# Kernel tuning notes

Hardware: AMD Instinct MI355X
Metric: run time of the kernel (lower is better)

## Reference

```python
import jax, jax.numpy as jnp
import numpy as np

TOP_K = 5


def setup_inputs() -> dict:
    key = jax.random.key(0)
    k1, k2 = jax.random.split(key)
    batch, n_attr, feat_dim = 4096, 64000, 512  # 1000 classes x 64 attrs
    image_features = jax.random.normal(k1, (batch, feat_dim), dtype=jnp.float32)
    # raw (unnormalized) attribute concept features, flattened to (n_attr, feat_dim)
    attr_features = jax.random.normal(k2, (n_attr, feat_dim), dtype=jnp.float32)
    return {"image_features": image_features, "attr_features": attr_features}


def reference(image_features, attr_features):
    # __init__: L2-normalize attribute features along feature dim
    attr_norm = attr_features / jnp.linalg.norm(attr_features, axis=-1, keepdims=True)
    # similarities: (batch, n_attr) dense dot-product matrix
    similarities = image_features @ attr_norm.T
    # top-k along attribute dim
    top_scores, top_indices = jax.lax.top_k(similarities, TOP_K)
    # gather selected attribute vectors: (batch, top_k, feat_dim)
    top_attr_features = attr_norm[top_indices]
    return (top_attr_features, top_scores)
```

## Files before the change

kernel.cpp:

```cpp
#include <hip/hip_runtime.h>
#include <float.h>

#define FEAT 512
#define TOPK 5
#define NSEL 16
#define BM 256
#define BN 256
#define BKT 64
#define NKT (FEAT / BKT)
#define ABYTES (BM * BKT)
#define BUFB (2 * ABYTES)
#define NCB 4

typedef __attribute__((ext_vector_type(4))) int i32x4;

__device__ __forceinline__ void gl_lds16(const void* g, void* lds) {
    __builtin_amdgcn_global_load_lds(
        (const __attribute__((address_space(1))) unsigned int*)g,
        (__attribute__((address_space(3))) unsigned int*)lds, 16, 0, 0);
}

__global__ __launch_bounds__(256) void quant_attr(
    const float* __restrict__ in, signed char* __restrict__ q,
    float* __restrict__ inv) {
    const int w = threadIdx.x >> 6, l = threadIdx.x & 63;
    const int row = blockIdx.x * 4 + w;
    const float4* p = reinterpret_cast<const float4*>(in) + (size_t)row * (FEAT / 4);
    const float4 v0 = p[l * 2], v1 = p[l * 2 + 1];
    float ss = v0.x * v0.x + v0.y * v0.y + v0.z * v0.z + v0.w * v0.w +
               v1.x * v1.x + v1.y * v1.y + v1.z * v1.z + v1.w * v1.w;
#pragma unroll
    for (int m = 1; m < 64; m <<= 1) ss += __shfl_xor(ss, m);
    const float iv = 1.0f / sqrtf(fmaxf(ss, 1e-30f));
    const float qs = iv * 300.0f;
    int qv[8];
    qv[0] = __float2int_rn(v0.x * qs); qv[1] = __float2int_rn(v0.y * qs);
    qv[2] = __float2int_rn(v0.z * qs); qv[3] = __float2int_rn(v0.w * qs);
    qv[4] = __float2int_rn(v1.x * qs); qv[5] = __float2int_rn(v1.y * qs);
    qv[6] = __float2int_rn(v1.z * qs); qv[7] = __float2int_rn(v1.w * qs);
#pragma unroll
    for (int j = 0; j < 8; ++j) qv[j] = min(127, max(-127, qv[j]));
    int2 st;
    st.x = (qv[0] & 255) | ((qv[1] & 255) << 8) | ((qv[2] & 255) << 16) |
           ((unsigned)(qv[3] & 255) << 24);
    st.y = (qv[4] & 255) | ((qv[5] & 255) << 8) | ((qv[6] & 255) << 16) |
           ((unsigned)(qv[7] & 255) << 24);
    *reinterpret_cast<int2*>(q + (size_t)row * FEAT + l * 8) = st;
    if (l == 0) inv[row] = iv;
}

__global__ __launch_bounds__(256) void quant_img(
    const float* __restrict__ in, signed char* __restrict__ q) {
    const int w = threadIdx.x >> 6, l = threadIdx.x & 63;
    const int row = blockIdx.x * 4 + w;
    const float4* p = reinterpret_cast<const float4*>(in) + (size_t)row * (FEAT / 4);
    const float4 v0 = p[l * 2], v1 = p[l * 2 + 1];
    float mx = fmaxf(fmaxf(fmaxf(fabsf(v0.x), fabsf(v0.y)), fmaxf(fabsf(v0.z), fabsf(v0.w))),
                     fmaxf(fmaxf(fabsf(v1.x), fabsf(v1.y)), fmaxf(fabsf(v1.z), fabsf(v1.w))));
#pragma unroll
    for (int m = 1; m < 64; m <<= 1) mx = fmaxf(mx, __shfl_xor(mx, m));
    mx = fmaxf(mx, 1e-20f);
    const float qs = 127.0f / mx;
    const int q0 = __float2int_rn(v0.x * qs), q1 = __float2int_rn(v0.y * qs);
    const int q2 = __float2int_rn(v0.z * qs), q3 = __float2int_rn(v0.w * qs);
    const int q4 = __float2int_rn(v1.x * qs), q5 = __float2int_rn(v1.y * qs);
    const int q6 = __float2int_rn(v1.z * qs), q7 = __float2int_rn(v1.w * qs);
    int2 st;
    st.x = (q0 & 255) | ((q1 & 255) << 8) | ((q2 & 255) << 16) | ((unsigned)(q3 & 255) << 24);
    st.y = (q4 & 255) | ((q5 & 255) << 8) | ((q6 & 255) << 16) | ((unsigned)(q7 & 255) << 24);
    *reinterpret_cast<int2*>(q + (size_t)row * FEAT + l * 8) = st;
}

__global__ __launch_bounds__(512, 2) void coarse_kernel(
    const signed char* __restrict__ attrQ, const signed char* __restrict__ imgQ,
    unsigned* __restrict__ cand, int nablk, int niblk) {
    __shared__ __align__(1024) char lds[3][BUFB];
    const int tid = threadIdx.x;

    const int cpx = gridDim.x >> 3;
    const int wg = ((int)blockIdx.x & 7) * cpx + ((int)blockIdx.x >> 3);
    const int ablock = wg / niblk;
    const int iblock = wg % niblk;

    const int w = tid >> 6, l = tid & 63;
    const int wr = w >> 2, wc = w & 3;
    const int lrow = l & 15, lg = l >> 4;

    const int srow = tid >> 2, sg = tid & 3;
    const int ssw = sg ^ ((srow ^ (srow >> 2)) & 3);
    const signed char* asrc = attrQ + (size_t)(ablock * BM + srow) * FEAT + (ssw << 4);
    const signed char* bsrc = imgQ + (size_t)(iblock * BN + srow) * FEAT + (ssw << 4);

    int a_off[8], b_off[4];
#pragma unroll
    for (int m = 0; m < 8; ++m) {
        const int r = wr * 128 + m * 16 + lrow;
        a_off[m] = r * BKT + ((lg ^ ((r ^ (r >> 2)) & 3)) << 4);
    }
#pragma unroll
    for (int n = 0; n < 4; ++n) {
        const int r = wc * 64 + n * 16 + lrow;
        b_off[n] = ABYTES + r * BKT + ((lg ^ ((r ^ (r >> 2)) & 3)) << 4);
    }

    i32x4 acc[8][4];
#pragma unroll
    for (int m = 0; m < 8; ++m)
#pragma unroll
        for (int n = 0; n < 4; ++n) acc[m][n] = (i32x4){0, 0, 0, 0};

#define STAGE(bufi, kt)                                                      \
    {                                                                        \
        char* d_ = &lds[bufi][tid * 16];                                     \
        gl_lds16(asrc + (kt) * BKT, d_);                                     \
        gl_lds16(asrc + (kt) * BKT + (size_t)128 * FEAT, d_ + 8192);         \
        gl_lds16(bsrc + (kt) * BKT, d_ + 16384);                             \
        gl_lds16(bsrc + (kt) * BKT + (size_t)128 * FEAT, d_ + 24576);        \
    }

    STAGE(0, 0);
    int cur = 0, nxt = 1;
#pragma unroll 1
    for (int t = 0; t < NKT; ++t) {
        if (t < NKT - 1) {
            STAGE(nxt, t + 1);
            asm volatile("s_waitcnt vmcnt(4)" ::: "memory");
        } else {
            asm volatile("s_waitcnt vmcnt(0)" ::: "memory");
        }
        __builtin_amdgcn_s_barrier();
        __builtin_amdgcn_sched_barrier(0);
        const char* buf = &lds[cur][0];
        i32x4 bF[4], aF[8];
#pragma unroll
        for (int n = 0; n < 4; ++n)
            bF[n] = *reinterpret_cast<const i32x4*>(buf + b_off[n]);
#pragma unroll
        for (int m = 0; m < 8; ++m)
            aF[m] = *reinterpret_cast<const i32x4*>(buf + a_off[m]);
        __builtin_amdgcn_s_setprio(1);
#pragma unroll
        for (int m = 0; m < 8; ++m)
#pragma unroll
            for (int n = 0; n < 4; ++n)
                acc[m][n] = __builtin_amdgcn_mfma_i32_16x16x64_i8(
                    aF[m], bF[n], acc[m][n], 0, 0, 0);
        __builtin_amdgcn_s_setprio(0);
        cur = (cur == 2) ? 0 : cur + 1;
        nxt = (nxt == 2) ? 0 : nxt + 1;
    }
#undef STAGE

    unsigned m1[4] = {0u, 0u, 0u, 0u}, m2[4] = {0u, 0u, 0u, 0u};
#pragma unroll
    for (int m = 0; m < 8; ++m)
#pragma unroll
        for (int r = 0; r < 4; ++r) {
            const int rowl = wr * 128 + m * 16 + lg * 4 + r;
            const unsigned idxc = 2047u - (unsigned)rowl;
#pragma unroll
            for (int n = 0; n < 4; ++n) {
                const unsigned p =
                    (((unsigned)(acc[m][n][r] + (1 << 23)) << 8) & 0xFFFFF800u) | idxc;
                m2[n] = max(m2[n], min(m1[n], p));
                m1[n] = max(m1[n], p);
            }
        }

    unsigned* scratch = reinterpret_cast<unsigned*>(&lds[0][0]);
#pragma unroll
    for (int n = 0; n < 4; ++n) {
        scratch[(w * 64 + l) * 8 + n * 2] = m1[n];
        scratch[(w * 64 + l) * 8 + n * 2 + 1] = m2[n];
    }
    __syncthreads();

    if (tid < BN) {
        const int wc2 = tid >> 6, cw = tid & 63;
        const int n = cw >> 4, lr = cw & 15;
        unsigned best[NCB] = {0u, 0u, 0u, 0u};
#pragma unroll
        for (int wr2 = 0; wr2 < 2; ++wr2)
#pragma unroll
            for (int lg2 = 0; lg2 < 4; ++lg2)
#pragma unroll
                for (int k = 0; k < 2; ++k) {
                    const unsigned p =
                        scratch[((wr2 * 4 + wc2) * 64 + lg2 * 16 + lr) * 8 + n * 2 + k];
                    if (p > best[NCB - 1]) {
                        best[NCB - 1] = p;
#pragma unroll
                        for (int x = NCB - 1; x > 0; --x)
                            if (best[x] > best[x - 1]) {
                                const unsigned t_ = best[x];
                                best[x] = best[x - 1]; best[x - 1] = t_;
                            }
                    }
                }
        const size_t base = ((size_t)(iblock * BN + tid) * nablk + ablock) * NCB;
#pragma unroll
        for (int j = 0; j < NCB; ++j) cand[base + j] = best[j];
    }
}

__global__ __launch_bounds__(64) void select16_kernel(
    const unsigned* __restrict__ cand, int* __restrict__ sel, int nablk) {
    const int row = blockIdx.x;
    const int l = threadIdx.x;
    const int ncand = nablk * NCB;
    const unsigned* cr = cand + (size_t)row * ncand;
    unsigned p[16]; int c[16];
#pragma unroll
    for (int j = 0; j < 16; ++j) {
        const int slot = l * 16 + j;
        if (slot < ncand) {
            const unsigned v = cr[slot];
            p[j] = v;
            c[j] = (slot / NCB) * BM + (2047 - (int)(v & 0x7FFu));
        } else { p[j] = 0u; c[j] = 0x7fffffff; }
    }
    int* out = sel + (size_t)row * NSEL;
    for (int r = 0; r < NSEL; ++r) {
        unsigned bp = 0u; int bc = 0x7fffffff;
#pragma unroll
        for (int j = 0; j < 16; ++j)
            if (p[j] > bp || (p[j] == bp && c[j] < bc)) { bp = p[j]; bc = c[j]; }
#pragma unroll
        for (int m = 1; m < 64; m <<= 1) {
            const unsigned op = __shfl_xor(bp, m);
            const int oc = __shfl_xor(bc, m);
            if (op > bp || (op == bp && oc < bc)) { bp = op; bc = oc; }
        }
        if (l == 0) out[r] = bc;
#pragma unroll
        for (int j = 0; j < 16; ++j)
            if (p[j] == bp && c[j] == bc) { p[j] = 0u; c[j] = 0x7fffffff; }
    }
}

__global__ __launch_bounds__(256) void rescore_kernel(
    const float* __restrict__ img, const float* __restrict__ attr,
    const float* __restrict__ inv, const int* __restrict__ sel,
    float* __restrict__ out_scores, int* __restrict__ final_i) {
    __shared__ float s_sc[NSEL];
    const int row = blockIdx.x;
    const int w = threadIdx.x >> 6, l = threadIdx.x & 63;
    const float4* ip = reinterpret_cast<const float4*>(img) + (size_t)row * (FEAT / 4);
    const float4 a0 = ip[l * 2], a1 = ip[l * 2 + 1];
#pragma unroll
    for (int q = 0; q < 4; ++q) {
        const int slot = w * 4 + q;
        const int ci = sel[(size_t)row * NSEL + slot];
        const float4* ap = reinterpret_cast<const float4*>(attr) + (size_t)ci * (FEAT / 4);
        const float4 b0 = ap[l * 2], b1 = ap[l * 2 + 1];
        float d = a0.x * b0.x + a0.y * b0.y + a0.z * b0.z + a0.w * b0.w +
                  a1.x * b1.x + a1.y * b1.y + a1.z * b1.z + a1.w * b1.w;
#pragma unroll
        for (int m = 1; m < 64; m <<= 1) d += __shfl_xor(d, m);
        if (l == 0) s_sc[slot] = d * inv[ci];
    }
    __syncthreads();
    if (threadIdx.x == 0) {
        float ts[TOPK]; int ti[TOPK];
#pragma unroll
        for (int j = 0; j < TOPK; ++j) { ts[j] = -FLT_MAX; ti[j] = 0x7fffffff; }
        for (int e = 0; e < NSEL; ++e) {
            const float sv = s_sc[e];
            const int iv = sel[(size_t)row * NSEL + e];
            if (sv > ts[4] || (sv == ts[4] && iv < ti[4])) {
                ts[4] = sv; ti[4] = iv;
#pragma unroll
                for (int x = 4; x > 0; --x)
                    if (ts[x] > ts[x - 1] || (ts[x] == ts[x - 1] && ti[x] < ti[x - 1])) {
                        const float tf = ts[x]; ts[x] = ts[x - 1]; ts[x - 1] = tf;
                        const int td = ti[x]; ti[x] = ti[x - 1]; ti[x - 1] = td;
                    }
            }
        }
#pragma unroll
        for (int j = 0; j < TOPK; ++j) {
            out_scores[(size_t)row * TOPK + j] = ts[j];
            final_i[(size_t)row * TOPK + j] = ti[j];
        }
    }
}

__global__ __launch_bounds__(128) void gather_kernel(
    const float* __restrict__ attr, const float* __restrict__ inv,
    const int* __restrict__ final_i, float* __restrict__ out0) {
    const int pair = blockIdx.x;
    const int fi = final_i[pair];
    const float sc = inv[fi];
    const float4 v =
        reinterpret_cast<const float4*>(attr)[(size_t)fi * (FEAT / 4) + threadIdx.x];
    float4 o;
    o.x = v.x * sc; o.y = v.y * sc; o.z = v.z * sc; o.w = v.w * sc;
    reinterpret_cast<float4*>(out0)[(size_t)pair * (FEAT / 4) + threadIdx.x] = o;
}

extern "C" void kernel_launch(void* const* d_in, const int* in_sizes, int n_in,
                              void* d_out, int out_size, void* d_ws, size_t ws_size,
                              hipStream_t stream) {
    const float* img = (const float*)d_in[0];
    const float* attr = (const float*)d_in[1];
    const int batch = in_sizes[0] / FEAT;
    const int nattr = in_sizes[1] / FEAT;
    const int nablk = nattr / BM;
    const int niblk = batch / BN;

    char* ws = (char*)d_ws;
    signed char* attrQ = (signed char*)ws; ws += (size_t)nattr * FEAT;
    signed char* imgQ = (signed char*)ws;  ws += (size_t)batch * FEAT;
    float* inv = (float*)ws;               ws += (size_t)nattr * 4;
    unsigned* cand = (unsigned*)ws;        ws += (size_t)batch * nablk * NCB * 4;
    int* sel = (int*)ws;                   ws += (size_t)batch * NSEL * 4;
    int* final_i = (int*)ws;               ws += (size_t)batch * TOPK * 4;

    float* out0 = (float*)d_out;
    float* out_scores = out0 + (size_t)batch * TOPK * FEAT;

    quant_attr<<<nattr / 4, 256, 0, stream>>>(attr, attrQ, inv);
    quant_img<<<batch / 4, 256, 0, stream>>>(img, imgQ);
    coarse_kernel<<<nablk * niblk, 512, 0, stream>>>(attrQ, imgQ, cand, nablk, niblk);
    select16_kernel<<<batch, 64, 0, stream>>>(cand, sel, nablk);
    rescore_kernel<<<batch, 256, 0, stream>>>(img, attr, inv, sel, out_scores, final_i);
    gather_kernel<<<batch * TOPK, 128, 0, stream>>>(attr, inv, final_i, out0);
}
```

Baseline: 282.2 us.

## Switch coarse GEMM to 32x32x32 int8 MFMA and fuse select/rescore/gather kernels

The coarse int8 GEMM now uses 32x32x32 MFMA tiles instead of 16x16x64, which cuts the number of MFMA issues and LDS fragment reads per k-step. Its LDS staging drops from triple to double buffering, with an extra barrier after each k-step, and a cross-half shuffle is added to the per-column top-2 reduction. Separately, the select16, rescore and gather kernels are merged into one per-row kernel that keeps the selected indices in shared memory, removing two launches and the global intermediates. The extra barrier may expose more load latency in the GEMM loop.

```diff
diff --git a/kernel.cpp b/kernel.cpp
--- a/kernel.cpp
+++ b/kernel.cpp
@@ -8,11 +8,12 @@
 #define BN 256
 #define BKT 64
 #define NKT (FEAT / BKT)
-#define ABYTES (BM * BKT)
-#define BUFB (2 * ABYTES)
+#define A_BYTES (BM * BKT)
+#define BUFB (2 * A_BYTES)
 #define NCB 4
 
 typedef __attribute__((ext_vector_type(4))) int i32x4;
+typedef __attribute__((ext_vector_type(16))) int i32x16;
 
 __device__ __forceinline__ void gl_lds16(const void* g, void* lds) {
     __builtin_amdgcn_global_load_lds(
@@ -74,7 +75,7 @@
 __global__ __launch_bounds__(512, 2) void coarse_kernel(
     const signed char* __restrict__ attrQ, const signed char* __restrict__ imgQ,
     unsigned* __restrict__ cand, int nablk, int niblk) {
-    __shared__ __align__(1024) char lds[3][BUFB];
+    __shared__ __align__(1024) char lds[2][BUFB];
     const int tid = threadIdx.x;
 
     const int cpx = gridDim.x >> 3;
@@ -84,30 +85,38 @@
 
     const int w = tid >> 6, l = tid & 63;
     const int wr = w >> 2, wc = w & 3;
-    const int lrow = l & 15, lg = l >> 4;
+    const int l31 = l & 31, lh = l >> 5;
 
     const int srow = tid >> 2, sg = tid & 3;
     const int ssw = sg ^ ((srow ^ (srow >> 2)) & 3);
     const signed char* asrc = attrQ + (size_t)(ablock * BM + srow) * FEAT + (ssw << 4);
     const signed char* bsrc = imgQ + (size_t)(iblock * BN + srow) * FEAT + (ssw << 4);
 
-    int a_off[8], b_off[4];
-#pragma unroll
-    for (int m = 0; m < 8; ++m) {
-        const int r = wr * 128 + m * 16 + lrow;
-        a_off[m] = r * BKT + ((lg ^ ((r ^ (r >> 2)) & 3)) << 4);
-    }
-#pragma unroll
-    for (int n = 0; n < 4; ++n) {
-        const int r = wc * 64 + n * 16 + lrow;
-        b_off[n] = ABYTES + r * BKT + ((lg ^ ((r ^ (r >> 2)) & 3)) << 4);
-    }
-
-    i32x4 acc[8][4];
-#pragma unroll
-    for (int m = 0; m < 8; ++m)
-#pragma unroll
-        for (int n = 0; n < 4; ++n) acc[m][n] = (i32x4){0, 0, 0, 0};
+    int a_off[4][2], b_off[2][2];
+#pragma unroll
+    for (int m = 0; m < 4; ++m)
+#pragma unroll
+        for (int ks = 0; ks < 2; ++ks) {
+            const int r = wr * 128 + m * 32 + l31;
+            const int g = ks * 2 + lh;
+            a_off[m][ks] = r * BKT + ((g ^ ((r ^ (r >> 2)) & 3)) << 4);
+        }
+#pragma unroll
+    for (int n = 0; n < 2; ++n)
+#pragma unroll
+        for (int ks = 0; ks < 2; ++ks) {
+            const int r = wc * 64 + n * 32 + l31;
+            const int g = ks * 2 + lh;
+            b_off[n][ks] = A_BYTES + r * BKT + ((g ^ ((r ^ (r >> 2)) & 3)) << 4);
+        }
+
+    i32x16 acc[4][2];
+#pragma unroll
+    for (int m = 0; m < 4; ++m)
+#pragma unroll
+        for (int n = 0; n < 2; ++n)
+#pragma unroll
+            for (int e = 0; e < 16; ++e) acc[m][n][e] = 0;
 
 #define STAGE(bufi, kt)                                                      \
     {                                                                        \
@@ -119,11 +128,11 @@
     }
 
     STAGE(0, 0);
-    int cur = 0, nxt = 1;
+    int cur = 0;
 #pragma unroll 1
     for (int t = 0; t < NKT; ++t) {
         if (t < NKT - 1) {
-            STAGE(nxt, t + 1);
+            STAGE(cur ^ 1, t + 1);
             asm volatile("s_waitcnt vmcnt(4)" ::: "memory");
         } else {
             asm volatile("s_waitcnt vmcnt(0)" ::: "memory");
@@ -131,126 +140,141 @@
         __builtin_amdgcn_s_barrier();
         __builtin_amdgcn_sched_barrier(0);
         const char* buf = &lds[cur][0];
-        i32x4 bF[4], aF[8];
-#pragma unroll
-        for (int n = 0; n < 4; ++n)
-            bF[n] = *reinterpret_cast<const i32x4*>(buf + b_off[n]);
-#pragma unroll
-        for (int m = 0; m < 8; ++m)
-            aF[m] = *reinterpret_cast<const i32x4*>(buf + a_off[m]);
+        i32x4 aF[4][2], bF[2][2];
+#pragma unroll
+        for (int n = 0; n < 2; ++n)
+#pragma unroll
+            for (int ks = 0; ks < 2; ++ks)
+                bF[n][ks] = *reinterpret_cast<const i32x4*>(buf + b_off[n][ks]);
+#pragma unroll
+        for (int m = 0; m < 4; ++m)
+#pragma unroll
+            for (int ks = 0; ks < 2; ++ks)
+                aF[m][ks] = *reinterpret_cast<const i32x4*>(buf + a_off[m][ks]);
         __builtin_amdgcn_s_setprio(1);
 #pragma unroll
-        for (int m = 0; m < 8; ++m)
-#pragma unroll
-            for (int n = 0; n < 4; ++n)
-                acc[m][n] = __builtin_amdgcn_mfma_i32_16x16x64_i8(
-                    aF[m], bF[n], acc[m][n], 0, 0, 0);
+        for (int ks = 0; ks < 2; ++ks)
+#pragma unroll
+            for (int m = 0; m < 4; ++m)
+#pragma unroll
+                for (int n = 0; n < 2; ++n)
+                    acc[m][n] = __builtin_amdgcn_mfma_i32_32x32x32_i8(
+                        aF[m][ks], bF[n][ks], acc[m][n], 0, 0, 0);
         __builtin_amdgcn_s_setprio(0);
-        cur = (cur == 2) ? 0 : cur + 1;
-        nxt = (nxt == 2) ? 0 : nxt + 1;
+        __builtin_amdgcn_sched_barrier(0);
+        __builtin_amdgcn_s_barrier();
+        cur ^= 1;
     }
 #undef STAGE
 
-    unsigned m1[4] = {0u, 0u, 0u, 0u}, m2[4] = {0u, 0u, 0u, 0u};
-#pragma unroll
-    for (int m = 0; m < 8; ++m)
-#pragma unroll
-        for (int r = 0; r < 4; ++r) {
-            const int rowl = wr * 128 + m * 16 + lg * 4 + r;
+    unsigned m1[2] = {0u, 0u}, m2[2] = {0u, 0u};
+#pragma unroll
+    for (int m = 0; m < 4; ++m)
+#pragma unroll
+        for (int reg = 0; reg < 16; ++reg) {
+            const int rowl = wr * 128 + m * 32 + (reg & 3) + 8 * (reg >> 2) + 4 * lh;
             const unsigned idxc = 2047u - (unsigned)rowl;
 #pragma unroll
-            for (int n = 0; n < 4; ++n) {
+            for (int n = 0; n < 2; ++n) {
                 const unsigned p =
-                    (((unsigned)(acc[m][n][r] + (1 << 23)) << 8) & 0xFFFFF800u) | idxc;
+                    (((unsigned)(acc[m][n][reg] + (1 << 23)) << 8) & 0xFFFFF800u) | idxc;
                 m2[n] = max(m2[n], min(m1[n], p));
                 m1[n] = max(m1[n], p);
             }
         }
 
+#pragma unroll
+    for (int n = 0; n < 2; ++n) {
+        const unsigned o1 = __shfl_xor(m1[n], 32);
+        const unsigned o2 = __shfl_xor(m2[n], 32);
+        m2[n] = max(max(m2[n], o2), min(m1[n], o1));
+        m1[n] = max(m1[n], o1);
+    }
+
+    __syncthreads();
     unsigned* scratch = reinterpret_cast<unsigned*>(&lds[0][0]);
-#pragma unroll
-    for (int n = 0; n < 4; ++n) {
-        scratch[(w * 64 + l) * 8 + n * 2] = m1[n];
-        scratch[(w * 64 + l) * 8 + n * 2 + 1] = m2[n];
+    if (lh == 0) {
+#pragma unroll
+        for (int n = 0; n < 2; ++n) {
+            scratch[(w * 64 + n * 32 + l31) * 2 + 0] = m1[n];
+            scratch[(w * 64 + n * 32 + l31) * 2 + 1] = m2[n];
+        }
     }
     __syncthreads();
 
     if (tid < BN) {
-        const int wc2 = tid >> 6, cw = tid & 63;
-        const int n = cw >> 4, lr = cw & 15;
+        const int wc2 = tid >> 6, lc = tid & 63;
         unsigned best[NCB] = {0u, 0u, 0u, 0u};
 #pragma unroll
         for (int wr2 = 0; wr2 < 2; ++wr2)
 #pragma unroll
-            for (int lg2 = 0; lg2 < 4; ++lg2)
-#pragma unroll
-                for (int k = 0; k < 2; ++k) {
-                    const unsigned p =
-                        scratch[((wr2 * 4 + wc2) * 64 + lg2 * 16 + lr) * 8 + n * 2 + k];
-                    if (p > best[NCB - 1]) {
-                        best[NCB - 1] = p;
-#pragma unroll
-                        for (int x = NCB - 1; x > 0; --x)
-                            if (best[x] > best[x - 1]) {
-                                const unsigned t_ = best[x];
-                                best[x] = best[x - 1]; best[x - 1] = t_;
-                            }
-                    }
+            for (int k = 0; k < 2; ++k) {
+                const unsigned p = scratch[((wr2 * 4 + wc2) * 64 + lc) * 2 + k];
+                if (p > best[NCB - 1]) {
+                    best[NCB - 1] = p;
+#pragma unroll
+                    for (int x = NCB - 1; x > 0; --x)
+                        if (best[x] > best[x - 1]) {
+                            const unsigned t_ = best[x];
+                            best[x] = best[x - 1]; best[x - 1] = t_;
+                        }
                 }
+            }
         const size_t base = ((size_t)(iblock * BN + tid) * nablk + ablock) * NCB;
 #pragma unroll
         for (int j = 0; j < NCB; ++j) cand[base + j] = best[j];
     }
 }
 
-__global__ __launch_bounds__(64) void select16_kernel(
-    const unsigned* __restrict__ cand, int* __restrict__ sel, int nablk) {
+__global__ __launch_bounds__(256) void final_kernel(
+    const float* __restrict__ img, const float* __restrict__ attr,
+    const float* __restrict__ inv, const unsigned* __restrict__ cand,
+    float* __restrict__ out0, float* __restrict__ out_scores, int nablk) {
+    __shared__ int s_sel[NSEL];
+    __shared__ float s_sc[NSEL];
+    __shared__ int s_fi[TOPK];
     const int row = blockIdx.x;
-    const int l = threadIdx.x;
-    const int ncand = nablk * NCB;
-    const unsigned* cr = cand + (size_t)row * ncand;
-    unsigned p[16]; int c[16];
-#pragma unroll
-    for (int j = 0; j < 16; ++j) {
-        const int slot = l * 16 + j;
-        if (slot < ncand) {
-            const unsigned v = cr[slot];
-            p[j] = v;
-            c[j] = (slot / NCB) * BM + (2047 - (int)(v & 0x7FFu));
-        } else { p[j] = 0u; c[j] = 0x7fffffff; }
-    }
-    int* out = sel + (size_t)row * NSEL;
-    for (int r = 0; r < NSEL; ++r) {
-        unsigned bp = 0u; int bc = 0x7fffffff;
-#pragma unroll
-        for (int j = 0; j < 16; ++j)
-            if (p[j] > bp || (p[j] == bp && c[j] < bc)) { bp = p[j]; bc = c[j]; }
-#pragma unroll
-        for (int m = 1; m < 64; m <<= 1) {
-            const unsigned op = __shfl_xor(bp, m);
-            const int oc = __shfl_xor(bc, m);
-            if (op > bp || (op == bp && oc < bc)) { bp = op; bc = oc; }
-        }
-        if (l == 0) out[r] = bc;
-#pragma unroll
-        for (int j = 0; j < 16; ++j)
-            if (p[j] == bp && c[j] == bc) { p[j] = 0u; c[j] = 0x7fffffff; }
-    }
-}
-
-__global__ __launch_bounds__(256) void rescore_kernel(
-    const float* __restrict__ img, const float* __restrict__ attr,
-    const float* __restrict__ inv, const int* __restrict__ sel,
-    float* __restrict__ out_scores, int* __restrict__ final_i) {
-    __shared__ float s_sc[NSEL];
-    const int row = blockIdx.x;
-    const int w = threadIdx.x >> 6, l = threadIdx.x & 63;
+    const int tid = threadIdx.x;
+    const int w = tid >> 6, l = tid & 63;
+
+    if (w == 0) {
+        const int ncand = nablk * NCB;
+        const unsigned* cr = cand + (size_t)row * ncand;
+        unsigned p[16]; int c[16];
+#pragma unroll
+        for (int j = 0; j < 16; ++j) {
+            const int slot = l * 16 + j;
+            if (slot < ncand) {
+                const unsigned v = cr[slot];
+                p[j] = v;
+                c[j] = (slot / NCB) * BM + (2047 - (int)(v & 0x7FFu));
+            } else { p[j] = 0u; c[j] = 0x7fffffff; }
+        }
+        for (int r = 0; r < NSEL; ++r) {
+            unsigned bp = 0u; int bc = 0x7fffffff;
+#pragma unroll
+            for (int j = 0; j < 16; ++j)
+                if (p[j] > bp || (p[j] == bp && c[j] < bc)) { bp = p[j]; bc = c[j]; }
+#pragma unroll
+            for (int m = 1; m < 64; m <<= 1) {
+                const unsigned op = __shfl_xor(bp, m);
+                const int oc = __shfl_xor(bc, m);
+                if (op > bp || (op == bp && oc < bc)) { bp = op; bc = oc; }
+            }
+            if (l == 0) s_sel[r] = bc;
+#pragma unroll
+            for (int j = 0; j < 16; ++j)
+                if (p[j] == bp && c[j] == bc) { p[j] = 0u; c[j] = 0x7fffffff; }
+        }
+    }
+    __syncthreads();
+
     const float4* ip = reinterpret_cast<const float4*>(img) + (size_t)row * (FEAT / 4);
     const float4 a0 = ip[l * 2], a1 = ip[l * 2 + 1];
 #pragma unroll
     for (int q = 0; q < 4; ++q) {
         const int slot = w * 4 + q;
-        const int ci = sel[(size_t)row * NSEL + slot];
+        const int ci = s_sel[slot];
         const float4* ap = reinterpret_cast<const float4*>(attr) + (size_t)ci * (FEAT / 4);
         const float4 b0 = ap[l * 2], b1 = ap[l * 2 + 1];
         float d = a0.x * b0.x + a0.y * b0.y + a0.z * b0.z + a0.w * b0.w +
@@ -260,13 +284,14 @@
         if (l == 0) s_sc[slot] = d * inv[ci];
     }
     __syncthreads();
-    if (threadIdx.x == 0) {
+
+    if (tid == 0) {
         float ts[TOPK]; int ti[TOPK];
 #pragma unroll
         for (int j = 0; j < TOPK; ++j) { ts[j] = -FLT_MAX; ti[j] = 0x7fffffff; }
         for (int e = 0; e < NSEL; ++e) {
             const float sv = s_sc[e];
-            const int iv = sel[(size_t)row * NSEL + e];
+            const int iv = s_sel[e];
             if (sv > ts[4] || (sv == ts[4] && iv < ti[4])) {
                 ts[4] = sv; ti[4] = iv;
 #pragma unroll
@@ -280,22 +305,20 @@
 #pragma unroll
         for (int j = 0; j < TOPK; ++j) {
             out_scores[(size_t)row * TOPK + j] = ts[j];
-            final_i[(size_t)row * TOPK + j] = ti[j];
-        }
-    }
-}
-
-__global__ __launch_bounds__(128) void gather_kernel(
-    const float* __restrict__ attr, const float* __restrict__ inv,
-    const int* __restrict__ final_i, float* __restrict__ out0) {
-    const int pair = blockIdx.x;
-    const int fi = final_i[pair];
-    const float sc = inv[fi];
-    const float4 v =
-        reinterpret_cast<const float4*>(attr)[(size_t)fi * (FEAT / 4) + threadIdx.x];
-    float4 o;
-    o.x = v.x * sc; o.y = v.y * sc; o.z = v.z * sc; o.w = v.w * sc;
-    reinterpret_cast<float4*>(out0)[(size_t)pair * (FEAT / 4) + threadIdx.x] = o;
+            s_fi[j] = ti[j];
+        }
+    }
+    __syncthreads();
+
+    for (int e = tid; e < TOPK * (FEAT / 4); e += 256) {
+        const int j = e >> 7, t4 = e & (FEAT / 4 - 1);
+        const int fi = s_fi[j];
+        const float sc = inv[fi];
+        const float4 v = reinterpret_cast<const float4*>(attr)[(size_t)fi * (FEAT / 4) + t4];
+        float4 o;
+        o.x = v.x * sc; o.y = v.y * sc; o.z = v.z * sc; o.w = v.w * sc;
+        reinterpret_cast<float4*>(out0)[((size_t)row * TOPK + j) * (FEAT / 4) + t4] = o;
+    }
 }
 
 extern "C" void kernel_launch(void* const* d_in, const int* in_sizes, int n_in,
@@ -313,8 +336,6 @@
     signed char* imgQ = (signed char*)ws;  ws += (size_t)batch * FEAT;
     float* inv = (float*)ws;               ws += (size_t)nattr * 4;
     unsigned* cand = (unsigned*)ws;        ws += (size_t)batch * nablk * NCB * 4;
-    int* sel = (int*)ws;                   ws += (size_t)batch * NSEL * 4;
-    int* final_i = (int*)ws;               ws += (size_t)batch * TOPK * 4;
 
     float* out0 = (float*)d_out;
     float* out_scores = out0 + (size_t)batch * TOPK * FEAT;
@@ -322,7 +343,6 @@
     quant_attr<<<nattr / 4, 256, 0, stream>>>(attr, attrQ, inv);
     quant_img<<<batch / 4, 256, 0, stream>>>(img, imgQ);
     coarse_kernel<<<nablk * niblk, 512, 0, stream>>>(attrQ, imgQ, cand, nablk, niblk);
-    select16_kernel<<<batch, 64, 0, stream>>>(cand, sel, nablk);
-    rescore_kernel<<<batch, 256, 0, stream>>>(img, attr, inv, sel, out_scores, final_i);
-    gather_kernel<<<batch * TOPK, 128, 0, stream>>>(attr, inv, final_i, out0);
-}
+    final_kernel<<<batch, 256, 0, stream>>>(img, attr, inv, cand, out0, out_scores,
+                                            nablk);
+}
```

Measured after the change: 307.5 us. 9.0% more time.
